# Kernel tuning notes

Measured on AMD Instinct MI355X. Metric: run time of the kernel, lower is better.

Reference implementation:

```python
import jax, jax.numpy as jnp
import numpy as np

N = 3072          # number of nodes
IN_DIM = 512
H = 8             # num_heads
D = 64            # out_dim per head
A = 8             # num_angles
CLAMP = 5.0


def setup_inputs() -> dict:
    key = jax.random.key(0)
    ks = jax.random.split(key, 9)
    HD = H * D
    return {
        "x": jax.random.normal(ks[0], (N, IN_DIM), jnp.float32),
        "node_rotation_angles": jax.random.normal(ks[1], (N, A), jnp.float32),
        "Wq": jax.random.normal(ks[2], (IN_DIM, HD), jnp.float32) * 0.05,
        "bq": jnp.zeros((HD,), jnp.float32),
        "Wk": jax.random.normal(ks[3], (IN_DIM, HD), jnp.float32) * 0.05,
        "bk": jnp.zeros((HD,), jnp.float32),
        "Wv": jax.random.normal(ks[4], (IN_DIM, HD), jnp.float32) * 0.05,
        "bv": jnp.zeros((HD,), jnp.float32),
        "S": jax.random.normal(ks[5], (A, HD // 2), jnp.float32),
    }


def reference(x, node_rotation_angles, Wq, bq, Wk, bk, Wv, bv, S):
    n = x.shape[0]
    # QKV projections -> [N, H, D]
    Qh = (x @ Wq + bq).reshape(n, H, D)
    Kh = (x @ Wk + bk).reshape(n, H, D)
    Vh = (x @ Wv + bv).reshape(n, H, D)

    # learned per-node rotation angles: [N, A] @ softmax(S, axis=1) -> [N, H*D/2]
    theta = node_rotation_angles @ jax.nn.softmax(S, axis=1)
    theta = jnp.repeat(theta, 2, axis=1).reshape(n, H, D)
    cos_pos = jnp.cos(theta)
    sin_pos = jnp.sin(theta)

    # torch.stack([-q_odd, q_even], dim=2).reshape -> concat of halves (faithful)
    q2 = jnp.concatenate([-Qh[..., 1::2], Qh[..., ::2]], axis=-1)
    k2 = jnp.concatenate([-Kh[..., 1::2], Kh[..., ::2]], axis=-1)
    Q = Qh * cos_pos + q2 * sin_pos
    K = Kh * cos_pos + k2 * sin_pos

    # faithful to original: raw .view() (reshape), NOT a transpose
    src = K.reshape(H, D, n)    # [H, D, N]
    dest = Q.reshape(H, n, D)   # [H, N, D]

    score = jnp.einsum("hnd,hdm->hnm", dest, src) / (D ** 0.5)
    score = jnp.clip(score, -CLAMP, CLAMP)
    attn = jax.nn.softmax(score, axis=-1)  # [H, N, N]

    # V uses a true transpose in the original
    msg = jnp.einsum("hnm,hmd->hnd", attn, jnp.swapaxes(Vh, 0, 1))
    return jnp.swapaxes(msg, 0, 1)  # [N, H, D]
```

## Files before the change

### kernel.cpp

```cpp
#include <hip/hip_runtime.h>

#define NN     3072
#define IND    512
#define NH     8
#define DH     64
#define HDTOT  512
#define NA     8
#define THALF  256
#define DN     196608
#define NZ     6

typedef float f32x4 __attribute__((ext_vector_type(4)));
typedef short bf16x8 __attribute__((ext_vector_type(8)));
typedef unsigned int u32x2 __attribute__((ext_vector_type(2)));

__device__ __forceinline__ unsigned short f2bf(float f) {
    union { float f; unsigned u; } a; a.f = f;
    unsigned u = a.u;
    return (unsigned short)((u + 0x7FFFu + ((u >> 16) & 1u)) >> 16);
}
__device__ __forceinline__ unsigned pack2(float a, float b) {
    union { float f; unsigned u; } ua, ub; ua.f = a; ub.f = b;
    unsigned ra = ua.u + 0x7FFFu + ((ua.u >> 16) & 1u);
    unsigned rb = ub.u + 0x7FFFu + ((ub.u >> 16) & 1u);
    return __builtin_amdgcn_perm(rb, ra, 0x07060302);
}
__device__ __forceinline__ float ubits2f(unsigned u) {
    union { unsigned u; float f; } c; c.u = u; return c.f;
}

__global__ __launch_bounds__(256) void k_prep(
    const float* __restrict__ S, const float* __restrict__ x,
    const float* __restrict__ Wq, const float* __restrict__ Wk,
    const float* __restrict__ Wv,
    float* __restrict__ SM, unsigned short* __restrict__ xb,
    unsigned short* __restrict__ WTb)
{
    __shared__ float sh[32 * 33];
    const int b = blockIdx.x, t = threadIdx.x;
    if (b == 0) {
        const int wvp = t >> 6;
        const int ln  = t & 63;
        for (int a = wvp; a < NA; a += 4) {
            float4 v = *reinterpret_cast<const float4*>(&S[a * THALF + ln * 4]);
            float mx = fmaxf(fmaxf(v.x, v.y), fmaxf(v.z, v.w));
            #pragma unroll
            for (int m = 1; m < 64; m <<= 1) mx = fmaxf(mx, __shfl_xor(mx, m));
            float e0 = __expf(v.x - mx), e1 = __expf(v.y - mx);
            float e2 = __expf(v.z - mx), e3 = __expf(v.w - mx);
            float s = (e0 + e1) + (e2 + e3);
            #pragma unroll
            for (int m = 1; m < 64; m <<= 1) s += __shfl_xor(s, m);
            float inv = 1.0f / s;
            float4 o; o.x = e0 * inv; o.y = e1 * inv; o.z = e2 * inv; o.w = e3 * inv;
            *reinterpret_cast<float4*>(&SM[a * THALF + ln * 4]) = o;
        }
    } else if (b <= 768) {
        const size_t base = ((size_t)(b - 1) * 256 + t) * 8;
        float4 v0 = *reinterpret_cast<const float4*>(&x[base]);
        float4 v1 = *reinterpret_cast<const float4*>(&x[base + 4]);
        uint4 w;
        w.x = pack2(v0.x, v0.y); w.y = pack2(v0.z, v0.w);
        w.z = pack2(v1.x, v1.y); w.w = pack2(v1.z, v1.w);
        *reinterpret_cast<uint4*>(&xb[base]) = w;
    } else {
        const int b2 = b - 769;
        const int kt = b2 & 15, nt = b2 >> 4;
        const int k0 = kt * 32, n0 = nt * 32;
        const float* __restrict__ W = (n0 < 512) ? Wq : (n0 < 1024 ? Wk : Wv);
        const int nc0 = n0 & 511;
        const int r = t >> 5, c = t & 31;
        #pragma unroll
        for (int i = 0; i < 4; ++i)
            sh[(r + i * 8) * 33 + c] = W[(size_t)(k0 + r + i * 8) * HDTOT + nc0 + c];
        __syncthreads();
        #pragma unroll
        for (int i = 0; i < 4; ++i) {
            const int nr = r + i * 8;
            WTb[(size_t)(n0 + nr) * IND + k0 + c] = f2bf(sh[c * 33 + nr]);
        }
    }
}

__global__ __launch_bounds__(256) void k_qkv_mfma(
    const unsigned short* __restrict__ xb,
    const unsigned short* __restrict__ WTb,
    const float* __restrict__ bq, const float* __restrict__ bk,
    const float* __restrict__ bv,
    const float* __restrict__ angles, const float* __restrict__ SM,
    unsigned short* __restrict__ Qb, unsigned short* __restrict__ KTb,
    unsigned short* __restrict__ VTb)
{
    __shared__ __align__(16) char lds[41472];
    char* At  = lds;
    char* Bt  = lds + 16384;
    float* Cs = (float*)lds;
    float* SMl = (float*)(lds + 33280);

    const int t = threadIdx.x;
    const int lane = t & 63;
    const int wv = t >> 6;
    const int wrow = wv >> 1, wcol = wv & 1;
    const int l15 = lane & 15, lg = lane >> 4;
    const int r8 = lane >> 3, c8 = lane & 7;

    const int m0 = blockIdx.x * 128;
    const int n0 = blockIdx.y * 64;
    const int mat = n0 >> 9;
    const int c0 = n0 & 511;

    if (mat < 2) {
        #pragma unroll
        for (int r = 0; r < 8; ++r) SMl[r * 256 + t] = SM[r * 256 + t];
    }

    f32x4 acc[4][2];
    #pragma unroll
    for (int mf = 0; mf < 4; ++mf)
        #pragma unroll
        for (int nf = 0; nf < 2; ++nf)
            acc[mf][nf] = (f32x4){0.f, 0.f, 0.f, 0.f};

    for (int kt = 0; kt < 8; ++kt) {
        __syncthreads();
        #pragma unroll
        for (int i = 0; i < 4; ++i) {
            const int row = wv * 32 + i * 8 + r8;
            const unsigned short* src =
                xb + (size_t)(m0 + row) * IND + kt * 64 + (c8 ^ (row & 7)) * 8;
            __builtin_amdgcn_global_load_lds(
                (const __attribute__((address_space(1))) unsigned int*)src,
                (__attribute__((address_space(3))) unsigned int*)(At + (wv * 32 + i * 8) * 128),
                16, 0, 0);
        }
        #pragma unroll
        for (int i = 0; i < 2; ++i) {
            const int row = wv * 16 + i * 8 + r8;
            const unsigned short* src =
                WTb + (size_t)(n0 + row) * IND + kt * 64 + (c8 ^ (row & 7)) * 8;
            __builtin_amdgcn_global_load_lds(
                (const __attribute__((address_space(1))) unsigned int*)src,
                (__attribute__((address_space(3))) unsigned int*)(Bt + (wv * 16 + i * 8) * 128),
                16, 0, 0);
        }
        __syncthreads();
        #pragma unroll
        for (int ks = 0; ks < 2; ++ks) {
            bf16x8 af[4], bfr[2];
            #pragma unroll
            for (int mf = 0; mf < 4; ++mf) {
                const int row = wrow * 64 + mf * 16 + l15;
                int off = row * 128 + ks * 64 + lg * 16;
                off ^= (row & 7) << 4;
                af[mf] = *reinterpret_cast<const bf16x8*>(At + off);
            }
            #pragma unroll
            for (int nf = 0; nf < 2; ++nf) {
                const int row = wcol * 32 + nf * 16 + l15;
                int off = row * 128 + ks * 64 + lg * 16;
                off ^= (row & 7) << 4;
                bfr[nf] = *reinterpret_cast<const bf16x8*>(Bt + off);
            }
            #pragma unroll
            for (int mf = 0; mf < 4; ++mf)
                #pragma unroll
                for (int nf = 0; nf < 2; ++nf)
                    acc[mf][nf] = __builtin_amdgcn_mfma_f32_16x16x32_bf16(
                        af[mf], bfr[nf], acc[mf][nf], 0, 0, 0);
        }
    }

    if (mat == 2) {
        #pragma unroll
        for (int nf = 0; nf < 2; ++nf) {
            const int cg = c0 + wcol * 32 + nf * 16 + l15;
            const float b = bv[cg];
            const int hV = cg >> 6, dd = cg & 63;
            #pragma unroll
            for (int mf = 0; mf < 4; ++mf) {
                const int nb = m0 + wrow * 64 + mf * 16 + lg * 4;
                u32x2 w;
                w.x = pack2(acc[mf][nf][0] + b, acc[mf][nf][1] + b);
                w.y = pack2(acc[mf][nf][2] + b, acc[mf][nf][3] + b);
                *reinterpret_cast<u32x2*>(&VTb[(size_t)hV * DN + (size_t)dd * NN + nb]) = w;
            }
        }
        return;
    }

    __syncthreads();
    const float* __restrict__ bsv = mat ? bk : bq;
    #pragma unroll
    for (int nf = 0; nf < 2; ++nf) {
        const int colc = wcol * 32 + nf * 16 + l15;
        const float b = bsv[c0 + colc];
        #pragma unroll
        for (int mf = 0; mf < 4; ++mf) {
            const int rb = wrow * 64 + mf * 16 + lg * 4;
            #pragma unroll
            for (int r = 0; r < 4; ++r)
                Cs[(rb + r) * 65 + colc] = acc[mf][nf][r] + b;
        }
    }
    __syncthreads();

    const int ni0 = (t & 15) * 4;
    const int rbase = (t >> 4) * 8;
    const int pidx = (c0 + ni0) >> 1;
    const int hK = m0 / 384;
    const float QS = 0.1803368801111204f;

    #pragma unroll
    for (int rr = 0; rr < 8; ++rr) {
        const int row = rbase + rr;
        const int n = m0 + row;
        const float4 a0 = *reinterpret_cast<const float4*>(&angles[n * NA]);
        const float4 a1 = *reinterpret_cast<const float4*>(&angles[n * NA + 4]);
        float th0, th1;
        th0 = a0.x * SMl[0 * 256 + pidx];
        th0 = fmaf(a0.y, SMl[1 * 256 + pidx], th0);
        th0 = fmaf(a0.z, SMl[2 * 256 + pidx], th0);
        th0 = fmaf(a0.w, SMl[3 * 256 + pidx], th0);
        th0 = fmaf(a1.x, SMl[4 * 256 + pidx], th0);
        th0 = fmaf(a1.y, SMl[5 * 256 + pidx], th0);
        th0 = fmaf(a1.z, SMl[6 * 256 + pidx], th0);
        th0 = fmaf(a1.w, SMl[7 * 256 + pidx], th0);
        th1 = a0.x * SMl[0 * 256 + pidx + 1];
        th1 = fmaf(a0.y, SMl[1 * 256 + pidx + 1], th1);
        th1 = fmaf(a0.z, SMl[2 * 256 + pidx + 1], th1);
        th1 = fmaf(a0.w, SMl[3 * 256 + pidx + 1], th1);
        th1 = fmaf(a1.x, SMl[4 * 256 + pidx + 1], th1);
        th1 = fmaf(a1.y, SMl[5 * 256 + pidx + 1], th1);
        th1 = fmaf(a1.z, SMl[6 * 256 + pidx + 1], th1);
        th1 = fmaf(a1.w, SMl[7 * 256 + pidx + 1], th1);
        float s0, c0f, s1, c1f;
        __sincosf(th0, &s0, &c0f);
        __sincosf(th1, &s1, &c1f);
        float o[4];
        #pragma unroll
        for (int cc = 0; cc < 4; ++cc) {
            const int d = ni0 + cc;
            const int pd = (d < 32) ? (2 * d + 1) : (2 * (d - 32));
            float own = Cs[row * 65 + d];
            float pv  = Cs[row * 65 + pd];
            float q2  = (d < 32) ? -pv : pv;
            float ct  = (cc < 2) ? c0f : c1f;
            float st  = (cc < 2) ? s0 : s1;
            o[cc] = own * ct + q2 * st;
        }
        if (mat == 0) {
            u32x2 w;
            w.x = pack2(o[0] * QS, o[1] * QS);
            w.y = pack2(o[2] * QS, o[3] * QS);
            *reinterpret_cast<u32x2*>(&Qb[(size_t)n * HDTOT + c0 + ni0]) = w;
        } else {
            const int nn = n - hK * 384;
            const int dk = nn / 6;
            const int jb = (nn - dk * 6) * 512 + c0 + ni0;
            #pragma unroll
            for (int cc = 0; cc < 4; ++cc)
                KTb[(size_t)hK * DN + (size_t)(jb + cc) * 64 + dk] = f2bf(o[cc]);
        }
    }
}

template<int TILES, bool PARTIAL>
__global__ __launch_bounds__(256) void k_attn(
    const unsigned short* __restrict__ Qb,
    const unsigned short* __restrict__ KTb,
    const unsigned short* __restrict__ VTb,
    float* __restrict__ outp, float* __restrict__ Dp)
{
    __shared__ __align__(16) char smem[32768];
    const int t = threadIdx.x;
    const int lane = t & 63;
    const int wv = t >> 6;
    char* ktl = smem;
    char* vtl = smem + 8192;
    char* ptw = smem + 16384 + wv * 4096;

    const int h = blockIdx.y;
    const int qbase = blockIdx.x * 128;
    const int z = blockIdx.z;
    const int jt0 = z * TILES;
    const int l15 = lane & 15;
    const int lg = lane >> 4;
    const int r8 = lane >> 3;
    const int c8 = lane & 7;

    const float CLP = 7.2134752044448170f;

    const int X  = (l15 & 7) << 4;
    const int A0 = l15 * 128 + ((lg * 16) ^ X);
    const int A1 = l15 * 128 + ((64 + lg * 16) ^ X);
    const int W0 = l15 * 128 + ((lg * 8) ^ X);
    const int W1 = l15 * 128 + ((32 + lg * 8) ^ X);
    const int W2 = l15 * 128 + ((64 + lg * 8) ^ X);
    const int W3 = l15 * 128 + ((96 + lg * 8) ^ X);

    bf16x8 qf[2][2];
    #pragma unroll
    for (int im = 0; im < 2; ++im)
        #pragma unroll
        for (int ks = 0; ks < 2; ++ks) {
            const int i = qbase + wv * 32 + im * 16 + l15;
            qf[im][ks] = *reinterpret_cast<const bf16x8*>(
                Qb + (size_t)h * DN + (size_t)i * 64 + ks * 32 + lg * 8);
        }

    f32x4 oacc[2][4];
    #pragma unroll
    for (int im = 0; im < 2; ++im)
        #pragma unroll
        for (int db = 0; db < 4; ++db)
            oacc[im][db] = (f32x4){0.f, 0.f, 0.f, 0.f};
    float dpart[2] = {0.f, 0.f};

    for (int jj = 0; jj < TILES; ++jj) {
        const int j0 = (jt0 + jj) * 64;
        #pragma unroll
        for (int cc = 0; cc < 2; ++cc) {
            const int row = wv * 16 + cc * 8 + r8;
            const int chunk = c8 ^ (row & 7);
            const unsigned short* srcK =
                KTb + (size_t)h * DN + (size_t)(j0 + row) * 64 + chunk * 8;
            __builtin_amdgcn_global_load_lds(
                (const __attribute__((address_space(1))) unsigned int*)srcK,
                (__attribute__((address_space(3))) unsigned int*)(ktl + (wv * 16 + cc * 8) * 128),
                16, 0, 0);
            const unsigned short* srcV =
                VTb + (size_t)h * DN + (size_t)row * NN + j0 + chunk * 8;
            __builtin_amdgcn_global_load_lds(
                (const __attribute__((address_space(1))) unsigned int*)srcV,
                (__attribute__((address_space(3))) unsigned int*)(vtl + (wv * 16 + cc * 8) * 128),
                16, 0, 0);
        }
        __syncthreads();

        f32x4 sac[2][4];
        #pragma unroll
        for (int im = 0; im < 2; ++im)
            #pragma unroll
            for (int jb = 0; jb < 4; ++jb)
                sac[im][jb] = (f32x4){0.f, 0.f, 0.f, 0.f};
        #pragma unroll
        for (int ks = 0; ks < 2; ++ks) {
            const int Aks = ks ? A1 : A0;
            bf16x8 kf[4];
            #pragma unroll
            for (int jb = 0; jb < 4; ++jb)
                kf[jb] = *reinterpret_cast<const bf16x8*>(ktl + Aks + jb * 2048);
            #pragma unroll
            for (int im = 0; im < 2; ++im)
                #pragma unroll
                for (int jb = 0; jb < 4; ++jb)
                    sac[im][jb] = __builtin_amdgcn_mfma_f32_16x16x32_bf16(
                        kf[jb], qf[im][ks], sac[im][jb], 0, 0, 0);
        }

        #pragma unroll
        for (int im = 0; im < 2; ++im) {
            #pragma unroll
            for (int jb = 0; jb < 4; ++jb) {
                float p[4];
                #pragma unroll
                for (int r = 0; r < 4; ++r) {
                    float sc = __builtin_amdgcn_fmed3f(sac[im][jb][r], -CLP, CLP);
                    p[r] = __builtin_amdgcn_exp2f(sc);
                }
                dpart[im] += (p[0] + p[1]) + (p[2] + p[3]);
                u32x2 w;
                w.x = pack2(p[0], p[1]);
                w.y = pack2(p[2], p[3]);
                const int aw = (jb == 0) ? W0 : (jb == 1) ? W1 : (jb == 2) ? W2 : W3;
                *reinterpret_cast<u32x2*>(ptw + aw + im * 2048) = w;
            }
        }

        bf16x8 pf[2][2];
        #pragma unroll
        for (int im = 0; im < 2; ++im)
            #pragma unroll
            for (int js = 0; js < 2; ++js)
                pf[im][js] = *reinterpret_cast<const bf16x8*>(
                    ptw + (js ? A1 : A0) + im * 2048);
        #pragma unroll
        for (int js = 0; js < 2; ++js) {
            const int Ajs = js ? A1 : A0;
            #pragma unroll
            for (int db = 0; db < 4; ++db) {
                bf16x8 vf = *reinterpret_cast<const bf16x8*>(vtl + Ajs + db * 2048);
                #pragma unroll
                for (int im = 0; im < 2; ++im)
                    oacc[im][db] = __builtin_amdgcn_mfma_f32_16x16x32_bf16(
                        vf, pf[im][js], oacc[im][db], 0, 0, 0);
            }
        }
        __syncthreads();
    }

    #pragma unroll
    for (int im = 0; im < 2; ++im) {
        float d = dpart[im];
        d += __shfl_xor(d, 16);
        d += __shfl_xor(d, 32);
        const int i = qbase + wv * 32 + im * 16 + l15;
        if (PARTIAL) {
            if (lg == 0) Dp[((size_t)z * NH + h) * NN + i] = d;
            unsigned short* Ob = (unsigned short*)outp;
            const size_t base = (((size_t)z * NH + h) * NN + i) * 64;
            #pragma unroll
            for (int db = 0; db < 4; ++db) {
                u32x2 w;
                w.x = pack2(oacc[im][db][0], oacc[im][db][1]);
                w.y = pack2(oacc[im][db][2], oacc[im][db][3]);
                *reinterpret_cast<u32x2*>(&Ob[base + db * 16 + lg * 4]) = w;
            }
        } else {
            const float inv = 1.0f / d;
            #pragma unroll
            for (int db = 0; db < 4; ++db) {
                float4 o;
                o.x = oacc[im][db][0] * inv; o.y = oacc[im][db][1] * inv;
                o.z = oacc[im][db][2] * inv; o.w = oacc[im][db][3] * inv;
                *reinterpret_cast<float4*>(
                    &outp[(size_t)i * HDTOT + h * DH + db * 16 + lg * 4]) = o;
            }
        }
    }
}

__global__ __launch_bounds__(256) void k_reduce(
    const unsigned short* __restrict__ Ob, const float* __restrict__ Dp,
    float* __restrict__ out, int nz)
{
    const int b  = blockIdx.x;
    const int t  = threadIdx.x;
    const int lo  = b & 7;
    const int mid = (b >> 3) % 6;
    const int hi  = b / 48;
    const int xq  = lo + 8 * mid;
    const int q   = hi * 256 + t;
    const int i   = xq * 64 + (q >> 7);
    const int h   = (q >> 4) & 7;
    const int dc  = q & 15;

    float o0 = 0.f, o1 = 0.f, o2 = 0.f, o3 = 0.f;
    float D = 0.f;
    for (int zz = 0; zz < nz; ++zz) {
        u32x2 v = *reinterpret_cast<const u32x2*>(
            &Ob[(((size_t)zz * NH + h) * NN + i) * 64 + dc * 4]);
        o0 += ubits2f(v.x << 16);
        o1 += ubits2f(v.x & 0xFFFF0000u);
        o2 += ubits2f(v.y << 16);
        o3 += ubits2f(v.y & 0xFFFF0000u);
        D += Dp[((size_t)zz * NH + h) * NN + i];
    }
    const float inv = 1.0f / D;
    float4 w;
    w.x = o0 * inv; w.y = o1 * inv; w.z = o2 * inv; w.w = o3 * inv;
    *reinterpret_cast<float4*>(&out[(size_t)i * HDTOT + h * 64 + dc * 4]) = w;
}

extern "C" void kernel_launch(void* const* d_in, const int* in_sizes, int n_in,
                              void* d_out, int out_size, void* d_ws, size_t ws_size,
                              hipStream_t stream)
{
    const float* x      = (const float*)d_in[0];
    const float* angles = (const float*)d_in[1];
    const float* Wq     = (const float*)d_in[2];
    const float* bq     = (const float*)d_in[3];
    const float* Wk     = (const float*)d_in[4];
    const float* bk     = (const float*)d_in[5];
    const float* Wv     = (const float*)d_in[6];
    const float* bv     = (const float*)d_in[7];
    const float* S      = (const float*)d_in[8];
    float* out = (float*)d_out;

    float* ws = (float*)d_ws;
    float* SM = ws;
    unsigned short* xb  = (unsigned short*)(ws + 4096);
    unsigned short* WTb = xb + (size_t)NN * IND;
    unsigned short* Qb  = WTb + (size_t)1536 * IND;
    unsigned short* KTb = Qb + (size_t)NN * HDTOT;
    unsigned short* VTb = KTb + (size_t)NN * HDTOT;
    unsigned short* Opart = VTb + (size_t)NN * HDTOT;
    float* Dpart = (float*)(Opart + (size_t)NZ * NH * NN * DH);
    const size_t need = (size_t)((char*)(Dpart + (size_t)NZ * NH * NN) - (char*)d_ws);

    k_prep<<<1537, 256, 0, stream>>>(S, x, Wq, Wk, Wv, SM, xb, WTb);
    k_qkv_mfma<<<dim3(24, 24), 256, 0, stream>>>(xb, WTb, bq, bk, bv,
                                                 angles, SM, Qb, KTb, VTb);
    if (ws_size >= need) {
        k_attn<48 / NZ, true><<<dim3(24, 8, NZ), 256, 0, stream>>>(Qb, KTb, VTb,
                                                                   (float*)Opart, Dpart);
        k_reduce<<<1536, 256, 0, stream>>>(Opart, Dpart, out, NZ);
    } else {
        k_attn<48, false><<<dim3(24, 8, 1), 256, 0, stream>>>(Qb, KTb, VTb, out, nullptr);
    }
}
```

Before: 69.30 us.

## Load K/V fragments directly from global memory, drop LDS staging and barriers

The attention kernel stops staging K and V tiles in shared memory via global_load_lds and instead has each wave read its MFMA operand fragments straight from global memory (relying on L1/L2 reuse across the four waves). This removes both per-tile __syncthreads and halves LDS usage, which may raise occupancy, and the tile loop is unrolled by two to expose more independent loads. The tradeoff is that every wave redundantly fetches the same K/V data from cache, with exposed global-load latency and less coalesced V accesses (strided by NN).

```diff
diff --git a/kernel.cpp b/kernel.cpp
--- a/kernel.cpp
+++ b/kernel.cpp
@@ -271,13 +271,11 @@
     const unsigned short* __restrict__ VTb,
     float* __restrict__ outp, float* __restrict__ Dp)
 {
-    __shared__ __align__(16) char smem[32768];
+    __shared__ __align__(16) char smem[16384];
     const int t = threadIdx.x;
     const int lane = t & 63;
     const int wv = t >> 6;
-    char* ktl = smem;
-    char* vtl = smem + 8192;
-    char* ptw = smem + 16384 + wv * 4096;
+    char* ptw = smem + wv * 4096;
 
     const int h = blockIdx.y;
     const int qbase = blockIdx.x * 128;
@@ -285,8 +283,6 @@
     const int jt0 = z * TILES;
     const int l15 = lane & 15;
     const int lg = lane >> 4;
-    const int r8 = lane >> 3;
-    const int c8 = lane & 7;
 
     const float CLP = 7.2134752044448170f;
 
@@ -298,6 +294,11 @@
     const int W2 = l15 * 128 + ((64 + lg * 8) ^ X);
     const int W3 = l15 * 128 + ((96 + lg * 8) ^ X);
 
+    const unsigned short* Kh = KTb + (size_t)h * DN;
+    const unsigned short* Vh = VTb + (size_t)h * DN;
+    const int kOff = l15 * 64 + lg * 8;
+    const size_t vOff = (size_t)l15 * NN + lg * 8;
+
     bf16x8 qf[2][2];
     #pragma unroll
     for (int im = 0; im < 2; ++im)
@@ -316,26 +317,11 @@
             oacc[im][db] = (f32x4){0.f, 0.f, 0.f, 0.f};
     float dpart[2] = {0.f, 0.f};
 
+    #pragma unroll 2
     for (int jj = 0; jj < TILES; ++jj) {
         const int j0 = (jt0 + jj) * 64;
-        #pragma unroll
-        for (int cc = 0; cc < 2; ++cc) {
-            const int row = wv * 16 + cc * 8 + r8;
-            const int chunk = c8 ^ (row & 7);
-            const unsigned short* srcK =
-                KTb + (size_t)h * DN + (size_t)(j0 + row) * 64 + chunk * 8;
-            __builtin_amdgcn_global_load_lds(
-                (const __attribute__((address_space(1))) unsigned int*)srcK,
-                (__attribute__((address_space(3))) unsigned int*)(ktl + (wv * 16 + cc * 8) * 128),
-                16, 0, 0);
-            const unsigned short* srcV =
-                VTb + (size_t)h * DN + (size_t)row * NN + j0 + chunk * 8;
-            __builtin_amdgcn_global_load_lds(
-                (const __attribute__((address_space(1))) unsigned int*)srcV,
-                (__attribute__((address_space(3))) unsigned int*)(vtl + (wv * 16 + cc * 8) * 128),
-                16, 0, 0);
-        }
-        __syncthreads();
+        const unsigned short* Kt = Kh + (size_t)j0 * 64 + kOff;
+        const unsigned short* Vt = Vh + j0 + vOff;
 
         f32x4 sac[2][4];
         #pragma unroll
@@ -345,11 +331,10 @@
                 sac[im][jb] = (f32x4){0.f, 0.f, 0.f, 0.f};
         #pragma unroll
         for (int ks = 0; ks < 2; ++ks) {
-            const int Aks = ks ? A1 : A0;
             bf16x8 kf[4];
             #pragma unroll
             for (int jb = 0; jb < 4; ++jb)
-                kf[jb] = *reinterpret_cast<const bf16x8*>(ktl + Aks + jb * 2048);
+                kf[jb] = *reinterpret_cast<const bf16x8*>(Kt + jb * 1024 + ks * 32);
             #pragma unroll
             for (int im = 0; im < 2; ++im)
                 #pragma unroll
@@ -386,17 +371,16 @@
                     ptw + (js ? A1 : A0) + im * 2048);
         #pragma unroll
         for (int js = 0; js < 2; ++js) {
-            const int Ajs = js ? A1 : A0;
             #pragma unroll
             for (int db = 0; db < 4; ++db) {
-                bf16x8 vf = *reinterpret_cast<const bf16x8*>(vtl + Ajs + db * 2048);
+                bf16x8 vf = *reinterpret_cast<const bf16x8*>(
+                    Vt + (size_t)db * (16 * NN) + js * 32);
                 #pragma unroll
                 for (int im = 0; im < 2; ++im)
                     oacc[im][db] = __builtin_amdgcn_mfma_f32_16x16x32_bf16(
                         vf, pf[im][js], oacc[im][db], 0, 0, 0);
             }
         }
-        __syncthreads();
     }
 
     #pragma unroll
```

After: 111.8 us. 1.61x slower.
